# Kernel optimization log

Hardware: AMD Instinct MI355X
Metric: run time of the kernel (lower is better)

Reference implementation:

```python
import jax, jax.numpy as jnp
import numpy as np

B = 4
S = 1024          # per-sequence length (equal for all sequences)
HQ = 32           # query heads
HK = 8            # kv heads (GQA)
D = 128           # head dim


def setup_inputs() -> dict:
    key = jax.random.key(0)
    k1, k2, k3 = jax.random.split(key, 3)
    total = B * S
    q = jax.random.normal(k1, (total, HQ, D), dtype=jnp.float32)
    k = jax.random.normal(k2, (total, HK, D), dtype=jnp.float32)
    v = jax.random.normal(k3, (total, HK, D), dtype=jnp.float32)
    cu = (jnp.arange(B + 1, dtype=jnp.int32) * S)
    return {
        "q": q, "k": k, "v": v,
        "cu_seqlens_q": cu, "cu_seqlens_k": cu,
        "max_seqlen_q": S, "max_seqlen_k": S,
    }


def reference(q, k, v, cu_seqlens_q, cu_seqlens_k, max_seqlen_q, max_seqlen_k):
    # Varlen causal GQA attention (prefill path of Attention.forward).
    # All sequences have equal length S = max_seqlen_q, so the packed varlen
    # layout is exactly a reshape to (B, S, H, D) -- same math as the
    # per-sequence Python loop in attention_varlen_func.
    total, Hq, Dh = q.shape
    Hk = k.shape[1]
    g = Hq // Hk                      # GQA group size
    Sq = int(max_seqlen_q)
    Bn = total // Sq
    scale = 1.0 / (Dh ** 0.5)

    qb = q.reshape(Bn, Sq, Hk, g, Dh)  # (B,S,Hk,g,D)
    kb = k.reshape(Bn, Sq, Hk, Dh)     # (B,S,Hk,D)
    vb = v.reshape(Bn, Sq, Hk, Dh)

    scores = jnp.einsum('bqhgd,bkhd->bhgqk', qb, kb) * scale  # (B,Hk,g,S,S)
    causal_mask = jnp.triu(jnp.ones((Sq, Sq), dtype=bool), k=1)
    scores = jnp.where(causal_mask, -jnp.inf, scores)
    attn = jax.nn.softmax(scores, axis=-1)
    out = jnp.einsum('bhgqk,bkhd->bqhgd', attn, vb)           # (B,S,Hk,g,D)
    return out.reshape(total, Hq, Dh)
```

## Files before the change

kernel.cpp:

```cpp
#include <hip/hip_runtime.h>
#include <hip/hip_bf16.h>
#include <stdint.h>


typedef __bf16 v8bf __attribute__((ext_vector_type(8)));
typedef __bf16 v4bf __attribute__((ext_vector_type(4)));
typedef float  v16f __attribute__((ext_vector_type(16)));

#define NB  4
#define NS  1024
#define NHQ 32
#define NHK 8
#define ND  128
#define BQ  128
#define BK  64

#define KOFF(r) (16*((r)>>3) + ((((r)>>2)&1)*4) + ((r)&3))

__global__ __launch_bounds__(256)
void prep(const float* __restrict__ kg, const float* __restrict__ vg,
          char* __restrict__ ws)
{
  const int tid = threadIdx.x;
  const int blk = blockIdx.x;
  if (blk < 4096) {
    int gid = blk * 256 + tid;
    int i  = gid & 31;
    int s  = (gid >> 5) & (NS - 1);
    int hk = (gid >> 15) & 7;
    int b  = gid >> 18;
    float4 f = *(const float4*)(kg + ((size_t)((b * NS + s) * NHK + hk)) * ND + 4 * i);
    v4bf kb;
    kb[0]=(__bf16)f.x; kb[1]=(__bf16)f.y; kb[2]=(__bf16)f.z; kb[3]=(__bf16)f.w;
    int t  = s >> 6;
    int c  = (s >> 5) & 1;
    int kk = s & 31;
    int mu = (kk & 3) + 4 * ((kk >> 3) & 1)
           + 8 * (2 * ((kk >> 4) & 1) + ((kk >> 2) & 1));
    int fidx  = c * 8 + (i >> 2);
    int halfb = (i >> 1) & 1;
    int byte  = fidx * 1024 + halfb * 512 + mu * 16 + ((4 * i) & 7) * 2;
    size_t tb = (size_t)((b * 8 + hk) * 16 + t) << 15;
    *(v4bf*)(ws + tb + byte) = kb;
  } else {
    int vid = (blk - 4096) * 256 + tid;
    int d  = vid & 127;
    int g  = (vid >> 7) & 7;
    int t  = (vid >> 10) & 15;
    int hk = (vid >> 14) & 7;
    int b  = vid >> 17;
    const float* vp = vg + ((size_t)((b * NS + t * 64 + g * 8) * NHK + hk)) * ND + d;
    v8bf w;
    #pragma unroll
    for (int e = 0; e < 8; ++e) w[e] = (__bf16)vp[(size_t)e * (NHK * ND)];
    int byte = (d * 8 + (g ^ ((d >> 1) & 7))) * 16;
    size_t tb = (size_t)((b * 8 + hk) * 16 + t) << 15;
    *(v8bf*)(ws + tb + 16384 + byte) = w;
  }
}

__global__ __launch_bounds__(256, 2)
void fattn(const float* __restrict__ qg, const char* __restrict__ kvg,
           float* __restrict__ og)
{
  __shared__ __align__(16) char  KV[2][32768];
  __shared__ __align__(16) float alq[4 * 32];

  const int tid  = threadIdx.x;
  const int lane = tid & 63;
  const int wave = tid >> 6;
  const int half = lane >> 5;
  const int l31  = lane & 31;

  const int bx = blockIdx.x;
  const int hk = bx & 7;
  const int t6 = bx >> 3;
  const int b  = t6 >> 4;
  const int m6 = t6 & 15;
  const int p  = m6 >> 2;
  const int h  = hk * 4 + (m6 & 3);

  const float scale = 0.12751879523604785f;
  const int kvtile = (b * 8 + hk) * 16;

  auto dma = [&](int t_, char* dst) {
    const char* src = kvg + ((size_t)(kvtile + t_) << 15);
    #pragma unroll
    for (int i = 0; i < 8; ++i) {
      int c = wave * 8 + i;
      __builtin_amdgcn_global_load_lds(
        (const __attribute__((address_space(1))) void*)(src + c * 1024 + lane * 16),
        (__attribute__((address_space(3))) void*)(dst + c * 1024),
        16, 0, 0);
    }
  };

  dma(0, KV[0]);
  int cur = 0;

  for (int ph = 0; ph < 2; ++ph) {
    const int qt = ph ? (7 - p) : p;
    const int wv = ph ? (3 - wave) : wave;
    const int q0 = qt * BQ;
    const int wqb = q0 + wv * 32;
    const int qglob = wqb + l31;
    const int ntiles = 2 * (qt + 1);

    v8bf qf[8];
    {
      const float* qp = qg + ((size_t)((b * NS + qglob) * NHQ + h)) * ND + half * 8;
      #pragma unroll
      for (int dM = 0; dM < 8; ++dM) {
        float4 f0 = *(const float4*)(qp + dM * 16);
        float4 f1 = *(const float4*)(qp + dM * 16 + 4);
        v8bf t;
        t[0]=(__bf16)(f0.x*scale); t[1]=(__bf16)(f0.y*scale);
        t[2]=(__bf16)(f0.z*scale); t[3]=(__bf16)(f0.w*scale);
        t[4]=(__bf16)(f1.x*scale); t[5]=(__bf16)(f1.y*scale);
        t[6]=(__bf16)(f1.z*scale); t[7]=(__bf16)(f1.w*scale);
        qf[dM] = t;
      }
    }

    v16f accO[4];
    #pragma unroll
    for (int dt = 0; dt < 4; ++dt)
      #pragma unroll
      for (int e = 0; e < 16; ++e) accO[dt][e] = 0.f;
    float m_run = -INFINITY, l_run = 0.f;

    for (int t = 0; t < ntiles; ++t) {
      const int k0 = t * BK;

      asm volatile("s_waitcnt vmcnt(0)" ::: "memory");
      __syncthreads();

      if (t + 1 < ntiles)      dma(t + 1, KV[cur ^ 1]);
      else if (ph == 0)        dma(0, KV[cur ^ 1]);

      if (k0 <= wqb + 31) {
        const char* ksr = KV[cur];
        const char* vtr = KV[cur] + 16384;
        v8bf ka0[8], ka1[8];
        #pragma unroll
        for (int f = 0; f < 8; ++f)
          ka0[f] = *(const v8bf*)(ksr + f * 1024 + lane * 16);
        #pragma unroll
        for (int f = 0; f < 8; ++f)
          ka1[f] = *(const v8bf*)(ksr + (f + 8) * 1024 + lane * 16);

        v16f s0, s1;
        #pragma unroll
        for (int e = 0; e < 16; ++e) { s0[e] = 0.f; s1[e] = 0.f; }
        __builtin_amdgcn_s_setprio(1);
        #pragma unroll
        for (int dM = 0; dM < 8; ++dM)
          s0 = __builtin_amdgcn_mfma_f32_32x32x16_bf16(ka0[dM], qf[dM], s0, 0, 0, 0);
        #pragma unroll
        for (int dM = 0; dM < 8; ++dM)
          s1 = __builtin_amdgcn_mfma_f32_32x32x16_bf16(ka1[dM], qf[dM], s1, 0, 0, 0);
        __builtin_amdgcn_s_setprio(0);
        if (k0 + BK > wqb) {
          #pragma unroll
          for (int r = 0; r < 16; ++r) {
            int key = k0 + KOFF(r) + half * 8;
            if (key > qglob)      s0[r] = -INFINITY;
            if (key + 32 > qglob) s1[r] = -INFINITY;
          }
        }
        float m0 = s0[0];
        #pragma unroll
        for (int r = 1; r < 16; ++r) m0 = fmaxf(m0, s0[r]);
        #pragma unroll
        for (int r = 0; r < 16; ++r) m0 = fmaxf(m0, s1[r]);
        m0 = fmaxf(m0, __shfl_xor(m0, 32));
        float mn = fmaxf(m_run, m0);
        float rs = 0.f;
        #pragma unroll
        for (int r = 0; r < 16; ++r) { float pp = exp2f(s0[r] - mn); s0[r] = pp; rs += pp; }
        #pragma unroll
        for (int r = 0; r < 16; ++r) { float pp = exp2f(s1[r] - mn); s1[r] = pp; rs += pp; }
        rs += __shfl_xor(rs, 32);
        if (__any(m0 > m_run)) {
          float al = exp2f(m_run - mn);
          if (half == 0) alq[wave * 32 + l31] = al;
          float4 alf[4];
          #pragma unroll
          for (int c = 0; c < 4; ++c)
            alf[c] = *(const float4*)(&alq[wave * 32 + 8 * c + 4 * half]);
          #pragma unroll
          for (int dt = 0; dt < 4; ++dt)
            #pragma unroll
            for (int r = 0; r < 16; ++r)
              accO[dt][r] *= ((const float*)&alf[r >> 2])[r & 3];
          l_run = l_run * al + rs;
        } else {
          l_run += rs;
        }
        m_run = mn;
        __builtin_amdgcn_s_setprio(1);
        #pragma unroll
        for (int C = 0; C < 2; ++C) {
          #pragma unroll
          for (int cp = 0; cp < 2; ++cp) {
            v8bf pf;
            #pragma unroll
            for (int e = 0; e < 8; ++e)
              pf[e] = (__bf16)(C == 0 ? s0[cp * 8 + e] : s1[cp * 8 + e]);
            int g = (C * 2 + cp) * 2 + half;
            #pragma unroll
            for (int dt = 0; dt < 4; ++dt) {
              int d = dt * 32 + l31;
              v8bf vb = *(const v8bf*)(vtr + (d * 8 + (g ^ ((l31 >> 1) & 7))) * 16);
              accO[dt] = __builtin_amdgcn_mfma_f32_32x32x16_bf16(pf, vb, accO[dt], 0, 0, 0);
            }
          }
        }
        __builtin_amdgcn_s_setprio(0);
      }
      cur ^= 1;
    }

    if (half == 0) alq[wave * 32 + l31] = 1.f / l_run;
    float4 invf[4];
    #pragma unroll
    for (int c = 0; c < 4; ++c)
      invf[c] = *(const float4*)(&alq[wave * 32 + 8 * c + 4 * half]);
    #pragma unroll
    for (int dt = 0; dt < 4; ++dt) {
      #pragma unroll
      for (int r = 0; r < 16; ++r) {
        int qrow = (r & 3) + 8 * (r >> 2) + 4 * half;
        float* op = og + ((size_t)((b * NS + wqb + qrow) * NHQ + h)) * ND;
        op[dt * 32 + l31] = accO[dt][r] * ((const float*)&invf[r >> 2])[r & 3];
      }
    }
  }
}

extern "C" void kernel_launch(void* const* d_in, const int* in_sizes, int n_in,
                              void* d_out, int out_size, void* d_ws, size_t ws_size,
                              hipStream_t stream) {
  const float* q = (const float*)d_in[0];
  const float* k = (const float*)d_in[1];
  const float* v = (const float*)d_in[2];
  float* out = (float*)d_out;
  char* ws = (char*)d_ws;
  prep<<<dim3(4096 + 2048), 256, 0, stream>>>(k, v, ws);
  fattn<<<dim3(NB * NHQ * 4), 256, 0, stream>>>(q, ws, out);
}
```

Baseline: 199.5 us.

## Run both causal q-tile phases concurrently in 512-thread blocks with shared KV stream

Each block now uses 8 waves: one group of four handles the light q-tile p and the other handles the heavy tile 7-p, both at once. A single KV stream of 2*(8-p) tiles is shared, replacing the two sequential passes that reloaded KV from tile 0. The block-to-head/tile mapping is rearranged to balance work. Softmax max and sum reductions become trees, and exp2f is replaced by raw v_exp_f32. The light group idles through the later tiles, and launch_bounds(512,4) tightens register limits, which may cause spills.

```diff
diff --git a/kernel.cpp b/kernel.cpp
--- a/kernel.cpp
+++ b/kernel.cpp
@@ -16,6 +16,10 @@
 #define BK  64
 
 #define KOFF(r) (16*((r)>>3) + ((((r)>>2)&1)*4) + ((r)&3))
+
+__device__ __forceinline__ float fexp2(float x) {
+  float r; asm("v_exp_f32 %0, %1" : "=v"(r) : "v"(x)); return r;
+}
 
 __global__ __launch_bounds__(256)
 void prep(const float* __restrict__ kg, const float* __restrict__ vg,
@@ -59,12 +63,12 @@
   }
 }
 
-__global__ __launch_bounds__(256, 2)
+__global__ __launch_bounds__(512, 4)
 void fattn(const float* __restrict__ qg, const char* __restrict__ kvg,
            float* __restrict__ og)
 {
   __shared__ __align__(16) char  KV[2][32768];
-  __shared__ __align__(16) float alq[4 * 32];
+  __shared__ __align__(16) float alq[8 * 32];
 
   const int tid  = threadIdx.x;
   const int lane = tid & 63;
@@ -72,13 +76,22 @@
   const int half = lane >> 5;
   const int l31  = lane & 31;
 
-  const int bx = blockIdx.x;
-  const int hk = bx & 7;
-  const int t6 = bx >> 3;
-  const int b  = t6 >> 4;
-  const int m6 = t6 & 15;
-  const int p  = m6 >> 2;
-  const int h  = hk * 4 + (m6 & 3);
+  const int bx  = blockIdx.x;
+  const int hk  = bx & 7;
+  const int u   = bx >> 3;
+  const int w   = u >> 5;
+  const int pb  = (u >> 3) & 3;
+  const int p   = w ? 3 - pb : pb;
+  const int rem = u & 7;
+  const int b   = rem >> 1;
+  const int h   = hk * 4 + ((rem & 1) * 2 + w);
+
+  const int grp = wave >> 2;
+  const int wv  = wave & 3;
+  const int qt  = grp ? (7 - p) : p;
+  const int wqb = qt * BQ + wv * 32;
+  const int qglob = wqb + l31;
+  const int nsteps = 2 * (8 - p);
 
   const float scale = 0.12751879523604785f;
   const int kvtile = (b * 8 + hk) * 16;
@@ -86,8 +99,8 @@
   auto dma = [&](int t_, char* dst) {
     const char* src = kvg + ((size_t)(kvtile + t_) << 15);
     #pragma unroll
-    for (int i = 0; i < 8; ++i) {
-      int c = wave * 8 + i;
+    for (int i = 0; i < 4; ++i) {
+      int c = wave * 4 + i;
       __builtin_amdgcn_global_load_lds(
         (const __attribute__((address_space(1))) void*)(src + c * 1024 + lane * 16),
         (__attribute__((address_space(3))) void*)(dst + c * 1024),
@@ -98,142 +111,142 @@
   dma(0, KV[0]);
   int cur = 0;
 
-  for (int ph = 0; ph < 2; ++ph) {
-    const int qt = ph ? (7 - p) : p;
-    const int wv = ph ? (3 - wave) : wave;
-    const int q0 = qt * BQ;
-    const int wqb = q0 + wv * 32;
-    const int qglob = wqb + l31;
-    const int ntiles = 2 * (qt + 1);
-
-    v8bf qf[8];
-    {
-      const float* qp = qg + ((size_t)((b * NS + qglob) * NHQ + h)) * ND + half * 8;
-      #pragma unroll
-      for (int dM = 0; dM < 8; ++dM) {
-        float4 f0 = *(const float4*)(qp + dM * 16);
-        float4 f1 = *(const float4*)(qp + dM * 16 + 4);
-        v8bf t;
-        t[0]=(__bf16)(f0.x*scale); t[1]=(__bf16)(f0.y*scale);
-        t[2]=(__bf16)(f0.z*scale); t[3]=(__bf16)(f0.w*scale);
-        t[4]=(__bf16)(f1.x*scale); t[5]=(__bf16)(f1.y*scale);
-        t[6]=(__bf16)(f1.z*scale); t[7]=(__bf16)(f1.w*scale);
-        qf[dM] = t;
+  v8bf qf[8];
+  {
+    const float* qp = qg + ((size_t)((b * NS + qglob) * NHQ + h)) * ND + half * 8;
+    #pragma unroll
+    for (int dM = 0; dM < 8; ++dM) {
+      float4 f0 = *(const float4*)(qp + dM * 16);
+      float4 f1 = *(const float4*)(qp + dM * 16 + 4);
+      v8bf t;
+      t[0]=(__bf16)(f0.x*scale); t[1]=(__bf16)(f0.y*scale);
+      t[2]=(__bf16)(f0.z*scale); t[3]=(__bf16)(f0.w*scale);
+      t[4]=(__bf16)(f1.x*scale); t[5]=(__bf16)(f1.y*scale);
+      t[6]=(__bf16)(f1.z*scale); t[7]=(__bf16)(f1.w*scale);
+      qf[dM] = t;
+    }
+  }
+
+  v16f accO[4];
+  #pragma unroll
+  for (int dt = 0; dt < 4; ++dt)
+    #pragma unroll
+    for (int e = 0; e < 16; ++e) accO[dt][e] = 0.f;
+  float m_run = -INFINITY, l_run = 0.f;
+
+  for (int t = 0; t < nsteps; ++t) {
+    const int k0 = t * BK;
+
+    asm volatile("s_waitcnt vmcnt(0)" ::: "memory");
+    __syncthreads();
+
+    if (t + 1 < nsteps) dma(t + 1, KV[cur ^ 1]);
+
+    if (k0 <= wqb + 31) {
+      const char* ksr = KV[cur];
+      const char* vtr = KV[cur] + 16384;
+      v8bf ka0[8], ka1[8];
+      #pragma unroll
+      for (int f = 0; f < 8; ++f)
+        ka0[f] = *(const v8bf*)(ksr + f * 1024 + lane * 16);
+      #pragma unroll
+      for (int f = 0; f < 8; ++f)
+        ka1[f] = *(const v8bf*)(ksr + (f + 8) * 1024 + lane * 16);
+
+      v16f s0, s1;
+      #pragma unroll
+      for (int e = 0; e < 16; ++e) { s0[e] = 0.f; s1[e] = 0.f; }
+      __builtin_amdgcn_s_setprio(1);
+      #pragma unroll
+      for (int dM = 0; dM < 8; ++dM)
+        s0 = __builtin_amdgcn_mfma_f32_32x32x16_bf16(ka0[dM], qf[dM], s0, 0, 0, 0);
+      #pragma unroll
+      for (int dM = 0; dM < 8; ++dM)
+        s1 = __builtin_amdgcn_mfma_f32_32x32x16_bf16(ka1[dM], qf[dM], s1, 0, 0, 0);
+      __builtin_amdgcn_s_setprio(0);
+      if (k0 + BK > wqb) {
+        #pragma unroll
+        for (int r = 0; r < 16; ++r) {
+          int key = k0 + KOFF(r) + half * 8;
+          if (key > qglob)      s0[r] = -INFINITY;
+          if (key + 32 > qglob) s1[r] = -INFINITY;
+        }
       }
-    }
-
-    v16f accO[4];
-    #pragma unroll
-    for (int dt = 0; dt < 4; ++dt)
-      #pragma unroll
-      for (int e = 0; e < 16; ++e) accO[dt][e] = 0.f;
-    float m_run = -INFINITY, l_run = 0.f;
-
-    for (int t = 0; t < ntiles; ++t) {
-      const int k0 = t * BK;
-
-      asm volatile("s_waitcnt vmcnt(0)" ::: "memory");
-      __syncthreads();
-
-      if (t + 1 < ntiles)      dma(t + 1, KV[cur ^ 1]);
-      else if (ph == 0)        dma(0, KV[cur ^ 1]);
-
-      if (k0 <= wqb + 31) {
-        const char* ksr = KV[cur];
-        const char* vtr = KV[cur] + 16384;
-        v8bf ka0[8], ka1[8];
-        #pragma unroll
-        for (int f = 0; f < 8; ++f)
-          ka0[f] = *(const v8bf*)(ksr + f * 1024 + lane * 16);
-        #pragma unroll
-        for (int f = 0; f < 8; ++f)
-          ka1[f] = *(const v8bf*)(ksr + (f + 8) * 1024 + lane * 16);
-
-        v16f s0, s1;
-        #pragma unroll
-        for (int e = 0; e < 16; ++e) { s0[e] = 0.f; s1[e] = 0.f; }
-        __builtin_amdgcn_s_setprio(1);
-        #pragma unroll
-        for (int dM = 0; dM < 8; ++dM)
-          s0 = __builtin_amdgcn_mfma_f32_32x32x16_bf16(ka0[dM], qf[dM], s0, 0, 0, 0);
-        #pragma unroll
-        for (int dM = 0; dM < 8; ++dM)
-          s1 = __builtin_amdgcn_mfma_f32_32x32x16_bf16(ka1[dM], qf[dM], s1, 0, 0, 0);
-        __builtin_amdgcn_s_setprio(0);
-        if (k0 + BK > wqb) {
+      float t16[16];
+      #pragma unroll
+      for (int i = 0; i < 16; ++i) t16[i] = fmaxf(s0[i], s1[i]);
+      #pragma unroll
+      for (int i = 0; i < 8; ++i) t16[i] = fmaxf(t16[i], t16[i + 8]);
+      #pragma unroll
+      for (int i = 0; i < 4; ++i) t16[i] = fmaxf(t16[i], t16[i + 4]);
+      float m0 = fmaxf(fmaxf(t16[0], t16[2]), fmaxf(t16[1], t16[3]));
+      m0 = fmaxf(m0, __shfl_xor(m0, 32));
+      float mn = fmaxf(m_run, m0);
+      #pragma unroll
+      for (int r = 0; r < 16; ++r) { s0[r] = fexp2(s0[r] - mn); }
+      #pragma unroll
+      for (int r = 0; r < 16; ++r) { s1[r] = fexp2(s1[r] - mn); }
+      float u16[16];
+      #pragma unroll
+      for (int i = 0; i < 16; ++i) u16[i] = s0[i] + s1[i];
+      #pragma unroll
+      for (int i = 0; i < 8; ++i) u16[i] = u16[i] + u16[i + 8];
+      #pragma unroll
+      for (int i = 0; i < 4; ++i) u16[i] = u16[i] + u16[i + 4];
+      float rs = (u16[0] + u16[2]) + (u16[1] + u16[3]);
+      rs += __shfl_xor(rs, 32);
+      if (__any(m0 > m_run)) {
+        float al = fexp2(m_run - mn);
+        if (half == 0) alq[wave * 32 + l31] = al;
+        float4 alf[4];
+        #pragma unroll
+        for (int c = 0; c < 4; ++c)
+          alf[c] = *(const float4*)(&alq[wave * 32 + 8 * c + 4 * half]);
+        #pragma unroll
+        for (int dt = 0; dt < 4; ++dt)
           #pragma unroll
-          for (int r = 0; r < 16; ++r) {
-            int key = k0 + KOFF(r) + half * 8;
-            if (key > qglob)      s0[r] = -INFINITY;
-            if (key + 32 > qglob) s1[r] = -INFINITY;
+          for (int r = 0; r < 16; ++r)
+            accO[dt][r] *= ((const float*)&alf[r >> 2])[r & 3];
+        l_run = l_run * al + rs;
+      } else {
+        l_run += rs;
+      }
+      m_run = mn;
+      __builtin_amdgcn_s_setprio(1);
+      #pragma unroll
+      for (int C = 0; C < 2; ++C) {
+        #pragma unroll
+        for (int cp = 0; cp < 2; ++cp) {
+          v8bf pf;
+          #pragma unroll
+          for (int e = 0; e < 8; ++e)
+            pf[e] = (__bf16)(C == 0 ? s0[cp * 8 + e] : s1[cp * 8 + e]);
+          int g = (C * 2 + cp) * 2 + half;
+          #pragma unroll
+          for (int dt = 0; dt < 4; ++dt) {
+            int d = dt * 32 + l31;
+            v8bf vb = *(const v8bf*)(vtr + (d * 8 + (g ^ ((l31 >> 1) & 7))) * 16);
+            accO[dt] = __builtin_amdgcn_mfma_f32_32x32x16_bf16(pf, vb, accO[dt], 0, 0, 0);
           }
         }
-        float m0 = s0[0];
-        #pragma unroll
-        for (int r = 1; r < 16; ++r) m0 = fmaxf(m0, s0[r]);
-        #pragma unroll
-        for (int r = 0; r < 16; ++r) m0 = fmaxf(m0, s1[r]);
-        m0 = fmaxf(m0, __shfl_xor(m0, 32));
-        float mn = fmaxf(m_run, m0);
-        float rs = 0.f;
-        #pragma unroll
-        for (int r = 0; r < 16; ++r) { float pp = exp2f(s0[r] - mn); s0[r] = pp; rs += pp; }
-        #pragma unroll
-        for (int r = 0; r < 16; ++r) { float pp = exp2f(s1[r] - mn); s1[r] = pp; rs += pp; }
-        rs += __shfl_xor(rs, 32);
-        if (__any(m0 > m_run)) {
-          float al = exp2f(m_run - mn);
-          if (half == 0) alq[wave * 32 + l31] = al;
-          float4 alf[4];
-          #pragma unroll
-          for (int c = 0; c < 4; ++c)
-            alf[c] = *(const float4*)(&alq[wave * 32 + 8 * c + 4 * half]);
-          #pragma unroll
-          for (int dt = 0; dt < 4; ++dt)
-            #pragma unroll
-            for (int r = 0; r < 16; ++r)
-              accO[dt][r] *= ((const float*)&alf[r >> 2])[r & 3];
-          l_run = l_run * al + rs;
-        } else {
-          l_run += rs;
-        }
-        m_run = mn;
-        __builtin_amdgcn_s_setprio(1);
-        #pragma unroll
-        for (int C = 0; C < 2; ++C) {
-          #pragma unroll
-          for (int cp = 0; cp < 2; ++cp) {
-            v8bf pf;
-            #pragma unroll
-            for (int e = 0; e < 8; ++e)
-              pf[e] = (__bf16)(C == 0 ? s0[cp * 8 + e] : s1[cp * 8 + e]);
-            int g = (C * 2 + cp) * 2 + half;
-            #pragma unroll
-            for (int dt = 0; dt < 4; ++dt) {
-              int d = dt * 32 + l31;
-              v8bf vb = *(const v8bf*)(vtr + (d * 8 + (g ^ ((l31 >> 1) & 7))) * 16);
-              accO[dt] = __builtin_amdgcn_mfma_f32_32x32x16_bf16(pf, vb, accO[dt], 0, 0, 0);
-            }
-          }
-        }
-        __builtin_amdgcn_s_setprio(0);
       }
-      cur ^= 1;
-    }
-
-    if (half == 0) alq[wave * 32 + l31] = 1.f / l_run;
-    float4 invf[4];
-    #pragma unroll
-    for (int c = 0; c < 4; ++c)
-      invf[c] = *(const float4*)(&alq[wave * 32 + 8 * c + 4 * half]);
-    #pragma unroll
-    for (int dt = 0; dt < 4; ++dt) {
-      #pragma unroll
-      for (int r = 0; r < 16; ++r) {
-        int qrow = (r & 3) + 8 * (r >> 2) + 4 * half;
-        float* op = og + ((size_t)((b * NS + wqb + qrow) * NHQ + h)) * ND;
-        op[dt * 32 + l31] = accO[dt][r] * ((const float*)&invf[r >> 2])[r & 3];
-      }
+      __builtin_amdgcn_s_setprio(0);
+    }
+    cur ^= 1;
+  }
+
+  if (half == 0) alq[wave * 32 + l31] = 1.f / l_run;
+  float4 invf[4];
+  #pragma unroll
+  for (int c = 0; c < 4; ++c)
+    invf[c] = *(const float4*)(&alq[wave * 32 + 8 * c + 4 * half]);
+  #pragma unroll
+  for (int dt = 0; dt < 4; ++dt) {
+    #pragma unroll
+    for (int r = 0; r < 16; ++r) {
+      int qrow = (r & 3) + 8 * (r >> 2) + 4 * half;
+      float* op = og + ((size_t)((b * NS + wqb + qrow) * NHQ + h)) * ND;
+      op[dt * 32 + l31] = accO[dt][r] * ((const float*)&invf[r >> 2])[r & 3];
     }
   }
 }
@@ -247,5 +260,5 @@
   float* out = (float*)d_out;
   char* ws = (char*)d_ws;
   prep<<<dim3(4096 + 2048), 256, 0, stream>>>(k, v, ws);
-  fattn<<<dim3(NB * NHQ * 4), 256, 0, stream>>>(q, ws, out);
-}
+  fattn<<<dim3(NB * NHQ * 4), 512, 0, stream>>>(q, ws, out);
+}
```

Result: slower. 391.3 us (+96.2%).

## Use fixed-offset lazy softmax rescaling with post-PV overflow correction

Applied to the files above, without the earlier changes.

Replaces the per-tile online-softmax max reduction with a fixed running offset (starting at 8). Exponentials are computed with raw v_exp_f32 before the PV MFMAs, and the row max and sum are checked afterward. Only when a probability exceeds 256 are the accumulator and the offset rescaled. K fragments are now loaded inside the MFMA loop to lower register pressure. This takes the max reduction off the critical path between the two matmuls, but it relies on scores staying within range. Tiles already multiplied into the accumulator with large probabilities are corrected afterward, which risks bf16 precision loss for extreme inputs.

```diff
diff --git a/kernel.cpp b/kernel.cpp
--- a/kernel.cpp
+++ b/kernel.cpp
@@ -16,6 +16,13 @@
 #define BK  64
 
 #define KOFF(r) (16*((r)>>3) + ((((r)>>2)&1)*4) + ((r)&3))
+
+__device__ __forceinline__ float fexp2(float x) {
+  float r; asm("v_exp_f32 %0, %1" : "=v"(r) : "v"(x)); return r;
+}
+__device__ __forceinline__ float flog2(float x) {
+  float r; asm("v_log_f32 %0, %1" : "=v"(r) : "v"(x)); return r;
+}
 
 __global__ __launch_bounds__(256)
 void prep(const float* __restrict__ kg, const float* __restrict__ vg,
@@ -127,7 +134,7 @@
     for (int dt = 0; dt < 4; ++dt)
       #pragma unroll
       for (int e = 0; e < 16; ++e) accO[dt][e] = 0.f;
-    float m_run = -INFINITY, l_run = 0.f;
+    float m_run = 8.0f, l_run = 0.f;
 
     for (int t = 0; t < ntiles; ++t) {
       const int k0 = t * BK;
@@ -141,24 +148,20 @@
       if (k0 <= wqb + 31) {
         const char* ksr = KV[cur];
         const char* vtr = KV[cur] + 16384;
-        v8bf ka0[8], ka1[8];
-        #pragma unroll
-        for (int f = 0; f < 8; ++f)
-          ka0[f] = *(const v8bf*)(ksr + f * 1024 + lane * 16);
-        #pragma unroll
-        for (int f = 0; f < 8; ++f)
-          ka1[f] = *(const v8bf*)(ksr + (f + 8) * 1024 + lane * 16);
-
         v16f s0, s1;
         #pragma unroll
         for (int e = 0; e < 16; ++e) { s0[e] = 0.f; s1[e] = 0.f; }
         __builtin_amdgcn_s_setprio(1);
         #pragma unroll
-        for (int dM = 0; dM < 8; ++dM)
-          s0 = __builtin_amdgcn_mfma_f32_32x32x16_bf16(ka0[dM], qf[dM], s0, 0, 0, 0);
-        #pragma unroll
-        for (int dM = 0; dM < 8; ++dM)
-          s1 = __builtin_amdgcn_mfma_f32_32x32x16_bf16(ka1[dM], qf[dM], s1, 0, 0, 0);
+        for (int dM = 0; dM < 8; ++dM) {
+          v8bf ka = *(const v8bf*)(ksr + dM * 1024 + lane * 16);
+          s0 = __builtin_amdgcn_mfma_f32_32x32x16_bf16(ka, qf[dM], s0, 0, 0, 0);
+        }
+        #pragma unroll
+        for (int dM = 0; dM < 8; ++dM) {
+          v8bf ka = *(const v8bf*)(ksr + (dM + 8) * 1024 + lane * 16);
+          s1 = __builtin_amdgcn_mfma_f32_32x32x16_bf16(ka, qf[dM], s1, 0, 0, 0);
+        }
         __builtin_amdgcn_s_setprio(0);
         if (k0 + BK > wqb) {
           #pragma unroll
@@ -168,36 +171,10 @@
             if (key + 32 > qglob) s1[r] = -INFINITY;
           }
         }
-        float m0 = s0[0];
-        #pragma unroll
-        for (int r = 1; r < 16; ++r) m0 = fmaxf(m0, s0[r]);
-        #pragma unroll
-        for (int r = 0; r < 16; ++r) m0 = fmaxf(m0, s1[r]);
-        m0 = fmaxf(m0, __shfl_xor(m0, 32));
-        float mn = fmaxf(m_run, m0);
-        float rs = 0.f;
-        #pragma unroll
-        for (int r = 0; r < 16; ++r) { float pp = exp2f(s0[r] - mn); s0[r] = pp; rs += pp; }
-        #pragma unroll
-        for (int r = 0; r < 16; ++r) { float pp = exp2f(s1[r] - mn); s1[r] = pp; rs += pp; }
-        rs += __shfl_xor(rs, 32);
-        if (__any(m0 > m_run)) {
-          float al = exp2f(m_run - mn);
-          if (half == 0) alq[wave * 32 + l31] = al;
-          float4 alf[4];
-          #pragma unroll
-          for (int c = 0; c < 4; ++c)
-            alf[c] = *(const float4*)(&alq[wave * 32 + 8 * c + 4 * half]);
-          #pragma unroll
-          for (int dt = 0; dt < 4; ++dt)
-            #pragma unroll
-            for (int r = 0; r < 16; ++r)
-              accO[dt][r] *= ((const float*)&alf[r >> 2])[r & 3];
-          l_run = l_run * al + rs;
-        } else {
-          l_run += rs;
-        }
-        m_run = mn;
+        #pragma unroll
+        for (int r = 0; r < 16; ++r) s0[r] = fexp2(s0[r] - m_run);
+        #pragma unroll
+        for (int r = 0; r < 16; ++r) s1[r] = fexp2(s1[r] - m_run);
         __builtin_amdgcn_s_setprio(1);
         #pragma unroll
         for (int C = 0; C < 2; ++C) {
@@ -217,6 +194,31 @@
           }
         }
         __builtin_amdgcn_s_setprio(0);
+        float rs = 0.f, pm = 0.f;
+        #pragma unroll
+        for (int r = 0; r < 16; ++r) {
+          rs += s0[r] + s1[r];
+          pm = fmaxf(pm, fmaxf(s0[r], s1[r]));
+        }
+        rs += __shfl_xor(rs, 32);
+        pm = fmaxf(pm, __shfl_xor(pm, 32));
+        if (__builtin_expect(__any(pm > 256.f), 0)) {
+          float al = pm > 256.f ? 1.f / pm : 1.f;
+          if (half == 0) alq[wave * 32 + l31] = al;
+          float4 alf[4];
+          #pragma unroll
+          for (int c = 0; c < 4; ++c)
+            alf[c] = *(const float4*)(&alq[wave * 32 + 8 * c + 4 * half]);
+          #pragma unroll
+          for (int dt = 0; dt < 4; ++dt)
+            #pragma unroll
+            for (int r = 0; r < 16; ++r)
+              accO[dt][r] *= ((const float*)&alf[r >> 2])[r & 3];
+          l_run = (l_run + rs) * al;
+          m_run += (pm > 256.f) ? flog2(pm) : 0.f;
+        } else {
+          l_run += rs;
+        }
       }
       cur ^= 1;
     }
```

Result: faster. 192.3 us (-3.6%).
